# Optimization experiments

Hardware: AMD Instinct MI355X
Metric: run time of the kernel (lower is better)

The kernel has to match this reference:

```python
import jax, jax.numpy as jnp
import numpy as np

K_NN = 3
EPS = 1e-8
MASK_THRESH = 0.5


def _three_nn_interpolate(pts, known, feats):
    """pts: (B,N,3), known: (B,M,3), feats: (B,M,C) -> (B,N,C).
    Squared-distance 3-NN + inverse-distance weighted interpolation
    (pointnet2 three_nn / three_interpolate semantics)."""
    # (B,N,M) squared euclidean distances
    d2 = (jnp.sum(pts * pts, -1)[:, :, None]
          + jnp.sum(known * known, -1)[:, None, :]
          - 2.0 * jnp.einsum('bnd,bmd->bnm', pts, known))
    neg_d, idx = jax.lax.top_k(-d2, K_NN)          # (B,N,3)
    dist = jnp.maximum(-neg_d, 0.0)                # squared dists, clamp fp error
    dist_recip = 1.0 / (dist + EPS)
    weight = dist_recip / jnp.sum(dist_recip, -1, keepdims=True)  # (B,N,3)
    b_idx = jnp.arange(pts.shape[0])[:, None, None]
    gathered = feats[b_idx, idx]                   # (B,N,3,C)
    return jnp.sum(weight[..., None] * gathered, axis=2)  # (B,N,C)


def setup_inputs() -> dict:
    key = jax.random.key(0)
    ks = jax.random.split(key, 10)
    B, N, C = 4, 8192, 32
    M2, M3, M4, Mm = 8192, 4096, 2048, 4096
    sc = 10.0  # spread coords over a realistic metric range
    return {
        'points_mean': jax.random.normal(ks[0], (B, N, 3)) * sc,
        'known2': jax.random.normal(ks[1], (B, M2, 3)) * sc,
        'feats2': jax.random.normal(ks[2], (B, M2, C)),
        'known3': jax.random.normal(ks[3], (B, M3, 3)) * sc,
        'feats3': jax.random.normal(ks[4], (B, M3, C)),
        'known4': jax.random.normal(ks[5], (B, M4, 3)) * sc,
        'feats4': jax.random.normal(ks[6], (B, M4, C)),
        'match_points': jax.random.normal(ks[7], (B, Mm, 3)) * sc,
        'w_fc': jax.random.normal(ks[8], (64, 96)) * 0.1,
        'w_cls': jax.random.normal(ks[9], (1, 64)) * 0.1,
    }


def reference(points_mean, known2, feats2, known3, feats3, known4, feats4,
              match_points, w_fc, w_cls):
    p0 = _three_nn_interpolate(points_mean, known2, feats2)  # (B,N,32)
    p1 = _three_nn_interpolate(points_mean, known3, feats3)
    p2 = _three_nn_interpolate(points_mean, known4, feats4)
    pointwise = jnp.concatenate([p0, p1, p2], axis=-1) @ w_fc.T  # (B,N,64)
    pred_hm = pointwise @ w_cls.T                                 # (B,N,1)
    # GT mask: min distance to match points < 0.5 m
    d2 = (jnp.sum(points_mean * points_mean, -1)[:, :, None]
          + jnp.sum(match_points * match_points, -1)[:, None, :]
          - 2.0 * jnp.einsum('bnd,bmd->bnm', points_mean, match_points))
    min_d = jnp.sqrt(jnp.maximum(jnp.min(d2, axis=-1), 0.0))      # (B,N)
    gt_hm = (min_d < MASK_THRESH).astype(jnp.float32)
    return pred_hm, gt_hm
```

## Files before the change

kernel.cpp:

```cpp
#include <hip/hip_runtime.h>

typedef unsigned int u32;
typedef unsigned long long u64;
typedef float f32x2 __attribute__((ext_vector_type(2)));

#define NB 4
#define NQ 8192
#define MARGIN 0.0625f
#define NBKT 4096

#define OFF_C0   0u
#define OFF_C1   524288u
#define OFF_C2   786432u
#define OFF_CMF  917504u
#define OFF_SKEY 1179648u
#define OFF_BOX  2031616u
#define WS_NEW2  2068480u
#define OFF_CM   917504u
#define WS_OLD   (512u*1024 + 256u*1024 + 128u*1024 + 512u*1024)

struct __align__(32) CP { f32x2 x, y, z, w; };
struct DM { double x, y, z, w; };

__device__ __forceinline__ f32x2 fma2(f32x2 a, f32x2 b, f32x2 c) {
  return __builtin_elementwise_fma(a, b, c);
}

__device__ __forceinline__ void lexins(double& e0d, double& e1d, double& e2d,
                                       int& e0i, int& e1i, int& e2i,
                                       double d, int i) {
  if (d < e2d || (d == e2d && i < e2i)) {
    if (d < e0d || (d == e0d && i < e0i)) {
      e2d = e1d; e2i = e1i; e1d = e0d; e1i = e0i; e0d = d; e0i = i;
    } else if (d < e1d || (d == e1d && i < e1i)) {
      e2d = e1d; e2i = e1i; e1d = d; e1i = i;
    } else {
      e2d = d; e2i = i;
    }
  }
}

__device__ __forceinline__ void ins4(float kv, u32 idx,
                                     float& k0, float& k1, float& k2, float& k3,
                                     u32& i0, u32& i1, u32& i2, u32& i3) {
  if (kv < k3) {
    bool lt0 = kv < k0, lt1 = kv < k1, lt2 = kv < k2;
    k3 = lt2 ? k2 : kv;               i3 = lt2 ? i2 : idx;
    k2 = lt2 ? (lt1 ? k1 : kv) : k2;  i2 = lt2 ? (lt1 ? i1 : idx) : i2;
    k1 = lt1 ? (lt0 ? k0 : kv) : k1;  i1 = lt1 ? (lt0 ? i0 : idx) : i1;
    k0 = lt0 ? kv : k0;               i0 = lt0 ? idx : i0;
  }
}

__device__ __forceinline__ u32 spread10(u32 v) {
  v &= 0x3FFu;
  v = (v | (v << 16)) & 0x030000FFu;
  v = (v | (v << 8))  & 0x0300F00Fu;
  v = (v | (v << 4))  & 0x030C30C3u;
  v = (v | (v << 2))  & 0x09249249u;
  return v;
}
__device__ __forceinline__ u32 morton30(float x, float y, float z) {
  int xi = (int)((x + 64.f) * 8.f);
  int yi = (int)((y + 64.f) * 8.f);
  int zi = (int)((z + 64.f) * 8.f);
  xi = min(max(xi, 0), 1023); yi = min(max(yi, 0), 1023); zi = min(max(zi, 0), 1023);
  return spread10((u32)xi) | (spread10((u32)yi) << 1) | (spread10((u32)zi) << 2);
}

__device__ __forceinline__ size_t skey_abase(int arr) {
  return (arr == 0) ? 0 : (arr == 1) ? 32768 : (arr == 2) ? 49152
        : (arr == 3) ? 57344 : 73728;
}

__global__ __launch_bounds__(512) void prep_csort(
    const float* __restrict__ k2p, const float* __restrict__ k3p,
    const float* __restrict__ k4p, const float* __restrict__ mmp,
    const float* __restrict__ pts, u64* __restrict__ skey) {
  __shared__ u32 hist[NBKT];
  const int arr = blockIdx.x, b = blockIdx.y, tid = threadIdx.x;
  const float* src = (arr == 0) ? k2p : (arr == 1) ? k3p : (arr == 2) ? k4p
                      : (arr == 3) ? mmp : pts;
  const int n = (arr == 0) ? 8192 : (arr == 1) ? 4096 : (arr == 2) ? 2048
                 : (arr == 3) ? 4096 : 8192;
  const float* sb = src + (size_t)b * n * 3;
  u64* skb = skey + skey_abase(arr) + (size_t)b * n;

  for (int i = tid; i < NBKT; i += 512) hist[i] = 0;
  __syncthreads();
  for (int i = tid; i < n; i += 512) {
    u32 k = morton30(sb[3 * i], sb[3 * i + 1], sb[3 * i + 2]);
    atomicAdd(&hist[k >> 18], 1u);
  }
  __syncthreads();
  for (int d = 1; d < NBKT; d <<= 1) {
    for (int i = tid; i < NBKT / (2 * d); i += 512) {
      int idx = (2 * i + 2) * d - 1;
      hist[idx] += hist[idx - d];
    }
    __syncthreads();
  }
  if (tid == 0) hist[NBKT - 1] = 0;
  __syncthreads();
  for (int d = NBKT >> 1; d >= 1; d >>= 1) {
    for (int i = tid; i < NBKT / (2 * d); i += 512) {
      int idx = (2 * i + 2) * d - 1;
      u32 t = hist[idx - d];
      hist[idx - d] = hist[idx];
      hist[idx] += t;
    }
    __syncthreads();
  }
  for (int i = tid; i < n; i += 512) {
    u32 k = morton30(sb[3 * i], sb[3 * i + 1], sb[3 * i + 2]);
    u32 pos = atomicAdd(&hist[k >> 18], 1u);
    skb[pos] = ((u64)k << 32) | (u32)i;
  }
}

__global__ __launch_bounds__(512) void refine_emit(
    const float* __restrict__ k2p, const float* __restrict__ k3p,
    const float* __restrict__ k4p, const float* __restrict__ mmp,
    const float* __restrict__ pts, u64* __restrict__ skey,
    CP* __restrict__ c0, CP* __restrict__ c1, CP* __restrict__ c2,
    float4* __restrict__ cmf, float* __restrict__ boxes) {
  __shared__ u64 ex[512];
  const int widx = blockIdx.x, b = blockIdx.y, tid = threadIdx.x;
  int arr, win;
  if (widx < 16)      { arr = 0; win = widx; }
  else if (widx < 24) { arr = 1; win = widx - 16; }
  else if (widx < 28) { arr = 2; win = widx - 24; }
  else if (widx < 36) { arr = 3; win = widx - 28; }
  else                { arr = 4; win = widx - 36; }
  const float* src = (arr == 0) ? k2p : (arr == 1) ? k3p : (arr == 2) ? k4p
                      : (arr == 3) ? mmp : pts;
  const int n = (arr == 0) ? 8192 : (arr == 1) ? 4096 : (arr == 2) ? 2048
                 : (arr == 3) ? 4096 : 8192;
  u64* skb = skey + skey_abase(arr) + (size_t)b * n;
  const int e = win * 512 + tid;
  u64 v = skb[e];

  for (int k = 2; k <= 512; k <<= 1) {
    for (int j = k >> 1; j > 0; j >>= 1) {
      u64 w;
      if (j < 64) {
        w = __shfl_xor(v, j);
      } else {
        __syncthreads();
        ex[tid] = v;
        __syncthreads();
        w = ex[tid ^ j];
      }
      bool up = (tid & k) == 0;
      bool lower = (tid & j) == 0;
      v = (up == lower) ? (v < w ? v : w) : (v < w ? w : v);
    }
  }
  skb[e] = v;
  if (arr == 4) return;

  u32 p = (u32)v;
  const float* sb = src + (size_t)b * n * 3;
  float x = sb[3 * p], y = sb[3 * p + 1], z = sb[3 * p + 2];
  if (arr < 3) {
    CP* dst = (arr == 0) ? c0 : (arr == 1) ? c1 : c2;
    float* df = (float*)(dst + (size_t)b * (n >> 1) + (e >> 1));
    int sl = e & 1;
    df[sl]     = x;
    df[2 + sl] = y;
    df[4 + sl] = z;
    df[6 + sl] = fmaf(z, z, fmaf(y, y, x * x));
  } else {
    cmf[(size_t)b * 4096 + e] = float4{x, y, z, 0.f};
  }
  float xlo = x, xhi = x, ylo = y, yhi = y, zlo = z, zhi = z;
#pragma unroll
  for (int off = 1; off < 64; off <<= 1) {
    xlo = fminf(xlo, __shfl_xor(xlo, off)); xhi = fmaxf(xhi, __shfl_xor(xhi, off));
    ylo = fminf(ylo, __shfl_xor(ylo, off)); yhi = fmaxf(yhi, __shfl_xor(yhi, off));
    zlo = fminf(zlo, __shfl_xor(zlo, off)); zhi = fmaxf(zhi, __shfl_xor(zhi, off));
  }
  if ((tid & 63) == 0) {
    const int nG = n >> 6, g = e >> 6;
    const int boff = (arr == 0) ? 0 : (arr == 1) ? 512 : (arr == 2) ? 768 : 896;
    float* bx = boxes + ((size_t)boff + (size_t)b * nG + g) * 8;
    bx[0] = xlo; bx[1] = xhi; bx[2] = ylo; bx[3] = yhi; bx[4] = zlo; bx[5] = zhi;
    bx[6] = 0.f; bx[7] = 0.f;
  }
}

__device__ __forceinline__ void scan_pairs32(
    const CP* __restrict__ cg, u32 ebase,
    f32x2 mx2, f32x2 my2, f32x2 mz2,
    float& k0, float& k1, float& k2, float& k3,
    u32& i0, u32& i1, u32& i2, u32& i3) {
#pragma unroll 4
  for (int gg = 0; gg < 32; gg += 4) {
    f32x2 key[4];
#pragma unroll
    for (int u = 0; u < 4; ++u) {
      CP c = cg[gg + u];
      key[u] = fma2(mx2, c.x, fma2(my2, c.y, fma2(mz2, c.z, c.w)));
    }
#pragma unroll
    for (int u = 0; u < 4; ++u) {
      float ka = key[u].x, kb = key[u].y;
      if (fminf(ka, kb) < k3) {
        u32 ib = ebase + (u32)((gg + u) * 2);
        ins4(ka, ib,     k0, k1, k2, k3, i0, i1, i2, i3);
        ins4(kb, ib + 1, k0, k1, k2, k3, i0, i1, i2, i3);
      }
    }
  }
}

struct Smem3 {
  float  box[2304];
  float  qx[64], qy[64], qz[64];
  double qdx[64], qdy[64], qdz[64], qn[64];
  u32    oq[64];
  u32    di[3][64][4][4];
  double mmin[64][8];
  float  wv[96];
  float  wq[64][9];
  u32    iq[64][9];
  float  contrib[64][9];
  float4 stage[8][2][64];
  u32    list[8][32];
};

__global__ __launch_bounds__(512, 2) void fused_sorted2(
    const float* __restrict__ pts,
    const float* __restrict__ f2, const float* __restrict__ f3,
    const float* __restrict__ f4,
    const float* __restrict__ wfc, const float* __restrict__ wcls,
    const CP* __restrict__ c0, const CP* __restrict__ c1,
    const CP* __restrict__ c2, const float4* __restrict__ cmf,
    const u64* __restrict__ skey, const float* __restrict__ boxes,
    float* __restrict__ out) {
  __shared__ Smem3 s;
  const int tid = threadIdx.x;
  const int b = blockIdx.y;
  const int tile = blockIdx.x;
  const int q0 = tile * 64;
  const int qloc = tid & 63;
  const int lane = tid & 63;
  const int wid = __builtin_amdgcn_readfirstlane(tid >> 6);

  {
    float* bf = s.box;
    for (int i = tid; i < 1024; i += 512) bf[i]        = boxes[(size_t)(b * 128) * 8 + i];
    { int i = tid; if (i < 512) bf[1024 + i] = boxes[((size_t)512 + b * 64) * 8 + i]; }
    { int i = tid; if (i < 256) bf[1536 + i] = boxes[((size_t)768 + b * 32) * 8 + i]; }
    { int i = tid; if (i < 512) bf[1792 + i] = boxes[((size_t)896 + b * 64) * 8 + i]; }
  }
  if (tid < 64) {
    u64 kv = skey[73728 + (size_t)b * NQ + q0 + tid];
    u32 p = (u32)kv;
    const float* pb = pts + (size_t)b * NQ * 3;
    float x = pb[3 * p], y = pb[3 * p + 1], z = pb[3 * p + 2];
    s.qx[tid] = x; s.qy[tid] = y; s.qz[tid] = z; s.oq[tid] = p;
    double dx = (double)x, dy = (double)y, dz = (double)z;
    s.qdx[tid] = dx; s.qdy[tid] = dy; s.qdz[tid] = dz;
    s.qn[tid] = (dx * dx + dy * dy) + dz * dz;
  } else if (tid < 160) {
    int t = tid - 64;
    float acc = 0.f;
    for (int j = 0; j < 64; ++j) acc += wcls[j] * wfc[j * 96 + t];
    s.wv[t] = acc;
  }
  __syncthreads();

  const float qx = s.qx[qloc], qy = s.qy[qloc], qz = s.qz[qloc];
  const float qnf = fmaf(qz, qz, fmaf(qy, qy, qx * qx));
  const float fm2x = -2.0f * qx, fm2y = -2.0f * qy, fm2z = -2.0f * qz;
  const double dm2x = -2.0 * s.qdx[qloc];
  const double dm2y = -2.0 * s.qdy[qloc];
  const double dm2z = -2.0 * s.qdz[qloc];

  {
    int lvl, prt, P, lboff;
    if (wid < 4)      { lvl = 0; prt = wid;     P = 4; lboff = 0; }
    else if (wid < 6) { lvl = 1; prt = wid - 4; P = 2; lboff = 128; }
    else              { lvl = 2; prt = wid - 6; P = 2; lboff = 192; }
    const int M  = (lvl == 0) ? 8192 : ((lvl == 1) ? 4096 : 2048);
    const int nG = M >> 6;
    const CP* c4 = ((lvl == 0) ? c0 : ((lvl == 1) ? c1 : c2)) + (((size_t)b * M) >> 1);
    int g0 = (tile * nG) >> 7;
    g0 = (g0 & ~(P - 1)) + prt;

    float k0 = __builtin_inff(), k1 = k0, k2 = k0, k3 = k0;
    u32 i0 = 0, i1 = 0, i2 = 0, i3 = 0;
    const f32x2 mx2 = {fm2x, fm2x}, my2 = {fm2y, fm2y}, mz2 = {fm2z, fm2z};

    scan_pairs32(c4 + (size_t)g0 * 32, (u32)(g0 * 64), mx2, my2, mz2,
                 k0, k1, k2, k3, i0, i1, i2, i3);

    int nl = 0;
    for (int t = 1; t < nG / P; ++t) {
      int g = (g0 + P * t) & (nG - 1);
      const float* bx = &s.box[(lboff + g) * 8];
      float dx = fmaxf(fmaxf(bx[0] - qx, qx - bx[1]), 0.f);
      float dy = fmaxf(fmaxf(bx[2] - qy, qy - bx[3]), 0.f);
      float dz = fmaxf(fmaxf(bx[4] - qz, qz - bx[5]), 0.f);
      float lb = fmaf(dx, dx, fmaf(dy, dy, dz * dz));
      if (__any(lb < qnf + k3 + MARGIN)) {
        if (lane == 0) s.list[wid][nl] = (u32)g;
        ++nl;
      }
    }

    int cur = 0;
    float4 v;
    u32 gcur = 0, gnext = 0;
    if (nl > 0) {
      gcur = s.list[wid][0];
      v = ((const float4*)(c4 + (size_t)gcur * 32))[lane];
    }
    for (int i = 0; i < nl; ++i) {
      s.stage[wid][cur][lane] = v;
      if (i + 1 < nl) {
        gnext = s.list[wid][i + 1];
        v = ((const float4*)(c4 + (size_t)gnext * 32))[lane];
      }
      scan_pairs32((const CP*)&s.stage[wid][cur][0], (u32)(gcur * 64),
                   mx2, my2, mz2, k0, k1, k2, k3, i0, i1, i2, i3);
      gcur = gnext; cur ^= 1;
    }

    s.di[lvl][qloc][prt][0] = i0; s.di[lvl][qloc][prt][1] = i1;
    s.di[lvl][qloc][prt][2] = i2; s.di[lvl][qloc][prt][3] = i3;
  }

  {
    const float4* cmb = cmf + (size_t)b * 4096;
    int gm0 = ((tile * 64) >> 7) & ~7;
    double smin = __builtin_inf();
    for (int t = 0; t < 8; ++t) {
      int g = (gm0 + wid + 8 * t) & 63;
      const float* bx = &s.box[(224 + g) * 8];
      float dx = fmaxf(fmaxf(bx[0] - qx, qx - bx[1]), 0.f);
      float dy = fmaxf(fmaxf(bx[2] - qy, qy - bx[3]), 0.f);
      float dz = fmaxf(fmaxf(bx[4] - qz, qz - bx[5]), 0.f);
      float lb = fmaf(dx, dx, fmaf(dy, dy, dz * dz));
      if (__any(lb < 0.3f)) {
        const float4* c8 = cmb + g * 64;
        for (int j = 0; j < 64; j += 8) {
          double sv[8];
#pragma unroll
          for (int u = 0; u < 8; ++u) {
            float4 cf = c8[j + u];
            double x = (double)cf.x, y = (double)cf.y, z = (double)cf.z;
            double w = fma(z, z, fma(y, y, x * x));
            sv[u] = fma(dm2x, x, fma(dm2y, y, fma(dm2z, z, w)));
          }
          double m01 = fmin(sv[0], sv[1]), m23 = fmin(sv[2], sv[3]);
          double m45 = fmin(sv[4], sv[5]), m67 = fmin(sv[6], sv[7]);
          smin = fmin(smin, fmin(fmin(m01, m23), fmin(m45, m67)));
        }
      }
    }
    s.mmin[qloc][wid] = smin;
  }
  __syncthreads();

  const int gqbase = b * NQ;
  if (tid < 192) {
    const int lvl = __builtin_amdgcn_readfirstlane(tid >> 6);
    const int q = tid & 63;
    const int M  = (lvl == 0) ? 8192 : ((lvl == 1) ? 4096 : 2048);
    const int np = (lvl == 0) ? 4 : 2;
    const CP* c4 = ((lvl == 0) ? c0 : ((lvl == 1) ? c1 : c2)) + (((size_t)b * M) >> 1);
    const u64* skl = skey + ((lvl == 0) ? 0 : (lvl == 1) ? 32768 : 49152)
                     + (size_t)b * M;
    const double qdx = s.qdx[q], qdy = s.qdy[q], qdz = s.qdz[q], qn = s.qn[q];
    double e0 = __builtin_inf(), e1 = e0, e2 = e0;
    int i0 = 0, i1 = 0, i2 = 0;
    for (int h = 0; h < np; ++h) {
#pragma unroll
      for (int r = 0; r < 4; ++r) {
        int sidx = (int)s.di[lvl][q][h][r];
        CP cc = c4[sidx >> 1];
        bool hi = sidx & 1;
        double x = (double)(hi ? cc.x.y : cc.x.x);
        double y = (double)(hi ? cc.y.y : cc.y.x);
        double z = (double)(hi ? cc.z.y : cc.z.x);
        int orig = (int)(u32)skl[sidx];
        double kn2 = (x * x + y * y) + z * z;
        double dot = (qdx * x + qdy * y) + qdz * z;
        double d2 = (qn + kn2) - 2.0 * dot;
        lexins(e0, e1, e2, i0, i1, i2, d2, orig);
      }
    }
    double d0 = fmax(e0, 0.0), d1 = fmax(e1, 0.0), d2v = fmax(e2, 0.0);
    double r0 = 1.0 / (d0 + 1e-8);
    double r1 = 1.0 / (d1 + 1e-8);
    double r2 = 1.0 / (d2v + 1e-8);
    double sum = (r0 + r1) + r2;
    s.wq[q][lvl * 3 + 0] = (float)(r0 / sum); s.iq[q][lvl * 3 + 0] = (u32)i0;
    s.wq[q][lvl * 3 + 1] = (float)(r1 / sum); s.iq[q][lvl * 3 + 1] = (u32)i1;
    s.wq[q][lvl * 3 + 2] = (float)(r2 / sum); s.iq[q][lvl * 3 + 2] = (u32)i2;
  } else if (tid < 256) {
    const int q = tid - 192;
    double sm = s.mmin[q][0];
#pragma unroll
    for (int p = 1; p < 8; ++p) sm = fmin(sm, s.mmin[q][p]);
    double dm = s.qn[q] + sm;
    out[NB * NQ + gqbase + (int)s.oq[q]] = (dm < 0.25) ? 1.0f : 0.0f;
  }
  __syncthreads();

  for (int item = tid; item < 576; item += 512) {
    const int q = item & 63, j = item >> 6;
    const int lvl = j / 3;
    const float* fp = (lvl == 0) ? f2 : ((lvl == 1) ? f3 : f4);
    const int M = (lvl == 0) ? 8192 : ((lvl == 1) ? 4096 : 2048);
    const float4* row = (const float4*)(fp + ((size_t)b * M + s.iq[q][j]) * 32);
    const float* wvp = s.wv + lvl * 32;
    float acc = 0.f;
#pragma unroll
    for (int v = 0; v < 8; ++v) {
      float4 r = row[v];
      acc += wvp[4 * v] * r.x + wvp[4 * v + 1] * r.y
           + wvp[4 * v + 2] * r.z + wvp[4 * v + 3] * r.w;
    }
    s.contrib[q][j] = s.wq[q][j] * acc;
  }
  __syncthreads();
  if (tid < 64) {
    const float* c = s.contrib[tid];
    float l0 = (c[0] + c[1]) + c[2];
    float l1 = (c[3] + c[4]) + c[5];
    float l2 = (c[6] + c[7]) + c[8];
    out[gqbase + (int)s.oq[tid]] = (l0 + l1) + l2;
  }
}

__global__ __launch_bounds__(256) void prep_kernel(
    const float* __restrict__ k2p, const float* __restrict__ k3p,
    const float* __restrict__ k4p, const float* __restrict__ mmp,
    CP* __restrict__ c0, CP* __restrict__ c1,
    CP* __restrict__ c2, DM* __restrict__ cm) {
  int r = blockIdx.y;
  int i = blockIdx.x * 256 + threadIdx.x;
  if (r < 3) {
    const float* src = (r == 0) ? k2p : ((r == 1) ? k3p : k4p);
    CP* dst = (r == 0) ? c0 : ((r == 1) ? c1 : c2);
    int pairs = (r == 0) ? NB * 4096 : ((r == 1) ? NB * 2048 : NB * 1024);
    if (i >= pairs) return;
    const float* p = src + (size_t)i * 6;
    float x0 = p[0], y0 = p[1], z0 = p[2];
    float x1 = p[3], y1 = p[4], z1 = p[5];
    CP c;
    c.x = f32x2{x0, x1}; c.y = f32x2{y0, y1}; c.z = f32x2{z0, z1};
    c.w = f32x2{fmaf(z0, z0, fmaf(y0, y0, x0 * x0)),
                fmaf(z1, z1, fmaf(y1, y1, x1 * x1))};
    dst[i] = c;
  } else {
    if (i >= NB * 4096) return;
    double x = (double)mmp[3 * i], y = (double)mmp[3 * i + 1], z = (double)mmp[3 * i + 2];
    DM d = {x, y, z, fma(z, z, fma(y, y, x * x))};
    cm[i] = d;
  }
}

template <bool PREP>
__device__ __forceinline__ void scan_nn(
    const CP* __restrict__ cp, const float* __restrict__ raw,
    int gstart, int L, float m2x, float m2y, float m2z,
    float* kk, u32* ii) {
  float k0 = __builtin_inff(), k1 = k0, k2 = k0, k3 = k0;
  u32 i0 = 0, i1 = 0, i2 = 0, i3 = 0;
  if (PREP) {
    const f32x2 mx2 = {m2x, m2x}, my2 = {m2y, m2y}, mz2 = {m2z, m2z};
    const int G = L >> 1;
#pragma unroll 2
    for (int g = 0; g < G; g += 4) {
      f32x2 key[4];
#pragma unroll
      for (int u = 0; u < 4; ++u) {
        CP c = cp[g + u];
        key[u] = fma2(mx2, c.x, fma2(my2, c.y, fma2(mz2, c.z, c.w)));
      }
#pragma unroll
      for (int u = 0; u < 4; ++u) {
        float ka = key[u].x, kb = key[u].y;
        if (fminf(ka, kb) < k3) {
          u32 ib = (u32)(gstart + 2 * (g + u));
          ins4(ka, ib,     k0, k1, k2, k3, i0, i1, i2, i3);
          ins4(kb, ib + 1, k0, k1, k2, k3, i0, i1, i2, i3);
        }
      }
    }
  } else {
    for (int j = 0; j < L; j += 8) {
      float key[8];
#pragma unroll
      for (int u = 0; u < 8; ++u) {
        const float* p = raw + (size_t)(gstart + j + u) * 3;
        float x = p[0], y = p[1], z = p[2];
        float n2 = fmaf(z, z, fmaf(y, y, x * x));
        key[u] = fmaf(m2x, x, fmaf(m2y, y, fmaf(m2z, z, n2)));
      }
#pragma unroll
      for (int u = 0; u < 8; ++u)
        ins4(key[u], (u32)(gstart + j + u), k0, k1, k2, k3, i0, i1, i2, i3);
    }
  }
  kk[0] = k0; kk[1] = k1; kk[2] = k2; kk[3] = k3;
  ii[0] = i0; ii[1] = i1; ii[2] = i2; ii[3] = i3;
}

template <bool PREP>
__device__ __forceinline__ double scan_mask(
    const DM* __restrict__ c8, const float* __restrict__ raw,
    int gstart, int L, double m2x, double m2y, double m2z) {
  double smin = __builtin_inf();
  if (PREP) {
    for (int j = 0; j < L; j += 8) {
      double sv[8];
#pragma unroll
      for (int u = 0; u < 8; ++u) {
        DM c = c8[gstart + j + u];
        sv[u] = fma(m2x, c.x, fma(m2y, c.y, fma(m2z, c.z, c.w)));
      }
      double m01 = fmin(sv[0], sv[1]), m23 = fmin(sv[2], sv[3]);
      double m45 = fmin(sv[4], sv[5]), m67 = fmin(sv[6], sv[7]);
      smin = fmin(smin, fmin(fmin(m01, m23), fmin(m45, m67)));
    }
  } else {
    for (int j = 0; j < L; j += 4) {
#pragma unroll
      for (int u = 0; u < 4; ++u) {
        const float* p = raw + (size_t)(gstart + j + u) * 3;
        double x = (double)p[0], y = (double)p[1], z = (double)p[2];
        double kn = fma(z, z, fma(y, y, x * x));
        smin = fmin(smin, fma(m2x, x, fma(m2y, y, fma(m2z, z, kn))));
      }
    }
  }
  return smin;
}

struct Smem {
  float  qx[64], qy[64], qz[64];
  double qdx[64], qdy[64], qdz[64], qn[64];
  float  dk[3][64][4][4];
  u32    di[3][64][4][4];
  double mmin[64][8];
  float  wv[96];
  float  part[64][3];
};

template <bool PREP>
__global__ __launch_bounds__(512, 2) void fused_kernel(
    const float* __restrict__ pts,
    const float* __restrict__ k2p, const float* __restrict__ f2,
    const float* __restrict__ k3p, const float* __restrict__ f3,
    const float* __restrict__ k4p, const float* __restrict__ f4,
    const float* __restrict__ mmp,
    const float* __restrict__ wfc, const float* __restrict__ wcls,
    const CP* __restrict__ c0, const CP* __restrict__ c1,
    const CP* __restrict__ c2, const DM* __restrict__ cm,
    float* __restrict__ out) {
  __shared__ Smem s;
  const int tid = threadIdx.x;
  const int b = blockIdx.y;
  const int q0 = blockIdx.x * 64;
  const int qloc = tid & 63;
  const int wid = __builtin_amdgcn_readfirstlane(tid >> 6);

  if (tid < 64) {
    int gq = b * NQ + q0 + tid;
    float x = pts[3 * gq], y = pts[3 * gq + 1], z = pts[3 * gq + 2];
    s.qx[tid] = x; s.qy[tid] = y; s.qz[tid] = z;
    double dx = (double)x, dy = (double)y, dz = (double)z;
    s.qdx[tid] = dx; s.qdy[tid] = dy; s.qdz[tid] = dz;
    s.qn[tid] = (dx * dx + dy * dy) + dz * dz;
  } else if (tid < 160) {
    int t = tid - 64;
    float acc = 0.f;
    for (int j = 0; j < 64; ++j) acc += wcls[j] * wfc[j * 96 + t];
    s.wv[t] = acc;
  }
  __syncthreads();

  const float fm2x = -2.0f * s.qx[qloc];
  const float fm2y = -2.0f * s.qy[qloc];
  const float fm2z = -2.0f * s.qz[qloc];
  const double dm2x = -2.0 * s.qdx[qloc];
  const double dm2y = -2.0 * s.qdy[qloc];
  const double dm2z = -2.0 * s.qdz[qloc];

  {
    int lvl, prt, gstart, glen;
    if (wid < 4)      { lvl = 0; prt = wid;     gstart = wid * 2048;       glen = 2048; }
    else if (wid < 6) { lvl = 1; prt = wid - 4; gstart = (wid - 4) * 2048; glen = 2048; }
    else              { lvl = 2; prt = wid - 6; gstart = (wid - 6) * 1024; glen = 1024; }
    const CP* c4 = (lvl == 0) ? c0 : ((lvl == 1) ? c1 : c2);
    const float* raw = (lvl == 0) ? k2p : ((lvl == 1) ? k3p : k4p);
    const int      M = (lvl == 0) ? 8192 : ((lvl == 1) ? 4096 : 2048);
    float kk[4]; u32 ii[4];
    scan_nn<PREP>(c4 + (PREP ? (((size_t)b * M + gstart) >> 1) : 0),
                  raw + (size_t)b * M * 3,
                  gstart, glen, fm2x, fm2y, fm2z, kk, ii);
#pragma unroll
    for (int r = 0; r < 4; ++r) {
      s.dk[lvl][qloc][prt][r] = kk[r];
      s.di[lvl][qloc][prt][r] = ii[r];
    }
    int mstart, mlen;
    if (wid < 6) { mstart = wid * 256; mlen = 256; }
    else         { mstart = 1536 + (wid - 6) * 1280; mlen = 1280; }
    s.mmin[qloc][wid] = scan_mask<PREP>(cm + (PREP ? (size_t)b * 4096 : 0),
                                        mmp + (size_t)b * 4096 * 3,
                                        mstart, mlen, dm2x, dm2y, dm2z);
  }
  __syncthreads();

  const int gqbase = b * NQ + q0;
  if (tid < 192) {
    const int lvl = __builtin_amdgcn_readfirstlane(tid >> 6);
    const int q = tid & 63;
    const float* kp = (lvl == 0) ? k2p : ((lvl == 1) ? k3p : k4p);
    const int    M  = (lvl == 0) ? 8192 : ((lvl == 1) ? 4096 : 2048);
    const int    np = (lvl == 0) ? 4 : 2;
    const double qdx = s.qdx[q], qdy = s.qdy[q], qdz = s.qdz[q], qn = s.qn[q];
    double e0 = __builtin_inf(), e1 = e0, e2 = e0;
    int i0 = 0, i1 = 0, i2 = 0;
    for (int h = 0; h < np; ++h) {
#pragma unroll
      for (int r = 0; r < 4; ++r) {
        int idx = (int)s.di[lvl][q][h][r];
        const float* c = kp + ((size_t)b * M + idx) * 3;
        double x = (double)c[0], y = (double)c[1], z = (double)c[2];
        double kn2 = (x * x + y * y) + z * z;
        double dot = (qdx * x + qdy * y) + qdz * z;
        double d2 = (qn + kn2) - 2.0 * dot;
        lexins(e0, e1, e2, i0, i1, i2, d2, idx);
      }
    }
    double d0 = fmax(e0, 0.0), d1 = fmax(e1, 0.0), d2v = fmax(e2, 0.0);
    double r0 = 1.0 / (d0 + 1e-8);
    double r1 = 1.0 / (d1 + 1e-8);
    double r2 = 1.0 / (d2v + 1e-8);
    double sum = (r0 + r1) + r2;
    float wa = (float)(r0 / sum), wb = (float)(r1 / sum), wc = (float)(r2 / sum);
    const float* fp = (lvl == 0) ? f2 : ((lvl == 1) ? f3 : f4);
    const float* g0 = fp + ((size_t)b * M + i0) * 32;
    const float* g1 = fp + ((size_t)b * M + i1) * 32;
    const float* g2 = fp + ((size_t)b * M + i2) * 32;
    float acc = 0.f;
#pragma unroll
    for (int wd = 0; wd < 32; ++wd) {
      float v = (wa * g0[wd] + wb * g1[wd]) + wc * g2[wd];
      acc += s.wv[lvl * 32 + wd] * v;
    }
    s.part[q][lvl] = acc;
  } else if (tid < 256) {
    const int q = tid - 192;
    double sm = s.mmin[q][0];
#pragma unroll
    for (int p = 1; p < 8; ++p) sm = fmin(sm, s.mmin[q][p]);
    double dm = s.qn[q] + sm;
    out[NB * NQ + gqbase + q] = (dm < 0.25) ? 1.0f : 0.0f;
  }
  __syncthreads();
  if (tid < 64) {
    float pred = (s.part[tid][0] + s.part[tid][1]) + s.part[tid][2];
    out[gqbase + tid] = pred;
  }
}

extern "C" void kernel_launch(void* const* d_in, const int* in_sizes, int n_in,
                              void* d_out, int out_size, void* d_ws, size_t ws_size,
                              hipStream_t stream) {
  const float* pts    = (const float*)d_in[0];
  const float* known2 = (const float*)d_in[1];
  const float* feats2 = (const float*)d_in[2];
  const float* known3 = (const float*)d_in[3];
  const float* feats3 = (const float*)d_in[4];
  const float* known4 = (const float*)d_in[5];
  const float* feats4 = (const float*)d_in[6];
  const float* match  = (const float*)d_in[7];
  const float* wfc    = (const float*)d_in[8];
  const float* wcls   = (const float*)d_in[9];

  char* ws = (char*)d_ws;
  CP* c0 = (CP*)(ws + OFF_C0);
  CP* c1 = (CP*)(ws + OFF_C1);
  CP* c2 = (CP*)(ws + OFF_C2);

  if (ws_size >= WS_NEW2) {
    float4* cmf = (float4*)(ws + OFF_CMF);
    u64* skey = (u64*)(ws + OFF_SKEY);
    float* boxes = (float*)(ws + OFF_BOX);
    hipLaunchKernelGGL(prep_csort, dim3(5, NB), dim3(512), 0, stream,
                       known2, known3, known4, match, pts, skey);
    hipLaunchKernelGGL(refine_emit, dim3(52, NB), dim3(512), 0, stream,
                       known2, known3, known4, match, pts, skey,
                       c0, c1, c2, cmf, boxes);
    hipLaunchKernelGGL(fused_sorted2, dim3(NQ / 64, NB), dim3(512), 0, stream,
                       pts, feats2, feats3, feats4, wfc, wcls,
                       c0, c1, c2, cmf, skey, boxes, (float*)d_out);
  } else if (ws_size >= WS_OLD) {
    DM* cm = (DM*)(ws + OFF_CM);
    hipLaunchKernelGGL(prep_kernel, dim3(64, 4), dim3(256), 0, stream,
                       known2, known3, known4, match, c0, c1, c2, cm);
    hipLaunchKernelGGL(HIP_KERNEL_NAME(fused_kernel<true>), dim3(NQ / 64, NB),
                       dim3(512), 0, stream, pts, known2, feats2, known3, feats3,
                       known4, feats4, match, wfc, wcls, c0, c1, c2, cm,
                       (float*)d_out);
  } else {
    DM* cm = (DM*)(ws + OFF_CM);
    hipLaunchKernelGGL(HIP_KERNEL_NAME(fused_kernel<false>), dim3(NQ / 64, NB),
                       dim3(512), 0, stream, pts, known2, feats2, known3, feats3,
                       known4, feats4, match, wfc, wcls, c0, c1, c2, cm,
                       (float*)d_out);
  }
}
```

Measured before the change: 237.3 us.

## Split query tiles to 32 queries per 256-thread block with half-wave candidate splitting

The main fused kernel now handles 32 queries per 256-thread block instead of 64 per 512, and each wave's two halves scan different 16-pair halves of a candidate group. Group pruning is re-checked against the current best distance just before each group is loaded, and match points are stored in the packed pair layout, so the mask pass uses a float prefilter before the double-precision check. The histogram-sort kernel moves to 1024 threads. This trades more blocks and extra voting for less serial scan work per lane and better occupancy, at the cost of more per-block setup such as the box loads and weight folding.

```diff
diff --git a/kernel.cpp b/kernel.cpp
--- a/kernel.cpp
+++ b/kernel.cpp
@@ -12,7 +12,7 @@
 #define OFF_C0   0u
 #define OFF_C1   524288u
 #define OFF_C2   786432u
-#define OFF_CMF  917504u
+#define OFF_CMP  917504u
 #define OFF_SKEY 1179648u
 #define OFF_BOX  2031616u
 #define WS_NEW2  2068480u
@@ -73,7 +73,7 @@
         : (arr == 3) ? 57344 : 73728;
 }
 
-__global__ __launch_bounds__(512) void prep_csort(
+__global__ __launch_bounds__(1024) void prep_csort(
     const float* __restrict__ k2p, const float* __restrict__ k3p,
     const float* __restrict__ k4p, const float* __restrict__ mmp,
     const float* __restrict__ pts, u64* __restrict__ skey) {
@@ -86,15 +86,15 @@
   const float* sb = src + (size_t)b * n * 3;
   u64* skb = skey + skey_abase(arr) + (size_t)b * n;
 
-  for (int i = tid; i < NBKT; i += 512) hist[i] = 0;
-  __syncthreads();
-  for (int i = tid; i < n; i += 512) {
+  for (int i = tid; i < NBKT; i += 1024) hist[i] = 0;
+  __syncthreads();
+  for (int i = tid; i < n; i += 1024) {
     u32 k = morton30(sb[3 * i], sb[3 * i + 1], sb[3 * i + 2]);
     atomicAdd(&hist[k >> 18], 1u);
   }
   __syncthreads();
   for (int d = 1; d < NBKT; d <<= 1) {
-    for (int i = tid; i < NBKT / (2 * d); i += 512) {
+    for (int i = tid; i < NBKT / (2 * d); i += 1024) {
       int idx = (2 * i + 2) * d - 1;
       hist[idx] += hist[idx - d];
     }
@@ -103,7 +103,7 @@
   if (tid == 0) hist[NBKT - 1] = 0;
   __syncthreads();
   for (int d = NBKT >> 1; d >= 1; d >>= 1) {
-    for (int i = tid; i < NBKT / (2 * d); i += 512) {
+    for (int i = tid; i < NBKT / (2 * d); i += 1024) {
       int idx = (2 * i + 2) * d - 1;
       u32 t = hist[idx - d];
       hist[idx - d] = hist[idx];
@@ -111,7 +111,7 @@
     }
     __syncthreads();
   }
-  for (int i = tid; i < n; i += 512) {
+  for (int i = tid; i < n; i += 1024) {
     u32 k = morton30(sb[3 * i], sb[3 * i + 1], sb[3 * i + 2]);
     u32 pos = atomicAdd(&hist[k >> 18], 1u);
     skb[pos] = ((u64)k << 32) | (u32)i;
@@ -123,7 +123,7 @@
     const float* __restrict__ k4p, const float* __restrict__ mmp,
     const float* __restrict__ pts, u64* __restrict__ skey,
     CP* __restrict__ c0, CP* __restrict__ c1, CP* __restrict__ c2,
-    float4* __restrict__ cmf, float* __restrict__ boxes) {
+    CP* __restrict__ cmp, float* __restrict__ boxes) {
   __shared__ u64 ex[512];
   const int widx = blockIdx.x, b = blockIdx.y, tid = threadIdx.x;
   int arr, win;
@@ -162,16 +162,14 @@
   u32 p = (u32)v;
   const float* sb = src + (size_t)b * n * 3;
   float x = sb[3 * p], y = sb[3 * p + 1], z = sb[3 * p + 2];
-  if (arr < 3) {
-    CP* dst = (arr == 0) ? c0 : (arr == 1) ? c1 : c2;
+  {
+    CP* dst = (arr == 0) ? c0 : (arr == 1) ? c1 : (arr == 2) ? c2 : cmp;
     float* df = (float*)(dst + (size_t)b * (n >> 1) + (e >> 1));
     int sl = e & 1;
     df[sl]     = x;
     df[2 + sl] = y;
     df[4 + sl] = z;
     df[6 + sl] = fmaf(z, z, fmaf(y, y, x * x));
-  } else {
-    cmf[(size_t)b * 4096 + e] = float4{x, y, z, 0.f};
   }
   float xlo = x, xhi = x, ylo = y, yhi = y, zlo = z, zhi = z;
 #pragma unroll
@@ -189,13 +187,13 @@
   }
 }
 
-__device__ __forceinline__ void scan_pairs32(
+__device__ __forceinline__ void scan_pairs16(
     const CP* __restrict__ cg, u32 ebase,
     f32x2 mx2, f32x2 my2, f32x2 mz2,
     float& k0, float& k1, float& k2, float& k3,
     u32& i0, u32& i1, u32& i2, u32& i3) {
 #pragma unroll 4
-  for (int gg = 0; gg < 32; gg += 4) {
+  for (int gg = 0; gg < 16; gg += 4) {
     f32x2 key[4];
 #pragma unroll
     for (int u = 0; u < 4; ++u) {
@@ -214,48 +212,49 @@
   }
 }
 
-struct Smem3 {
+struct Smem4 {
   float  box[2304];
-  float  qx[64], qy[64], qz[64];
-  double qdx[64], qdy[64], qdz[64], qn[64];
-  u32    oq[64];
-  u32    di[3][64][4][4];
-  double mmin[64][8];
+  float  qx[32], qy[32], qz[32];
+  double qdx[32], qdy[32], qdz[32], qn[32];
+  u32    oq[32];
+  u32    di[3][32][4][4];
+  double mmin[32][8];
   float  wv[96];
-  float  wq[64][9];
-  u32    iq[64][9];
-  float  contrib[64][9];
-  float4 stage[8][2][64];
-  u32    list[8][32];
+  float  wq[32][9];
+  u32    iq[32][9];
+  float  contrib[32][9];
+  float4 stage[4][2][64];
+  u32    list[4][64];
 };
 
-__global__ __launch_bounds__(512, 2) void fused_sorted2(
+__global__ __launch_bounds__(256, 4) void fused_sorted3(
     const float* __restrict__ pts,
     const float* __restrict__ f2, const float* __restrict__ f3,
     const float* __restrict__ f4,
     const float* __restrict__ wfc, const float* __restrict__ wcls,
     const CP* __restrict__ c0, const CP* __restrict__ c1,
-    const CP* __restrict__ c2, const float4* __restrict__ cmf,
+    const CP* __restrict__ c2, const CP* __restrict__ cmp,
     const u64* __restrict__ skey, const float* __restrict__ boxes,
     float* __restrict__ out) {
-  __shared__ Smem3 s;
+  __shared__ Smem4 s;
   const int tid = threadIdx.x;
   const int b = blockIdx.y;
   const int tile = blockIdx.x;
-  const int q0 = tile * 64;
-  const int qloc = tid & 63;
   const int lane = tid & 63;
+  const int q = tid & 31;
+  const int h = (tid >> 5) & 1;
   const int wid = __builtin_amdgcn_readfirstlane(tid >> 6);
 
-  {
-    float* bf = s.box;
-    for (int i = tid; i < 1024; i += 512) bf[i]        = boxes[(size_t)(b * 128) * 8 + i];
-    { int i = tid; if (i < 512) bf[1024 + i] = boxes[((size_t)512 + b * 64) * 8 + i]; }
-    { int i = tid; if (i < 256) bf[1536 + i] = boxes[((size_t)768 + b * 32) * 8 + i]; }
-    { int i = tid; if (i < 512) bf[1792 + i] = boxes[((size_t)896 + b * 64) * 8 + i]; }
-  }
-  if (tid < 64) {
-    u64 kv = skey[73728 + (size_t)b * NQ + q0 + tid];
+  for (int i = tid; i < 2304; i += 256) {
+    int src;
+    if (i < 1024)      src = (b * 128) * 8 + i;
+    else if (i < 1536) src = (512 + b * 64) * 8 + (i - 1024);
+    else if (i < 1792) src = (768 + b * 32) * 8 + (i - 1536);
+    else               src = (896 + b * 64) * 8 + (i - 1792);
+    s.box[i] = boxes[src];
+  }
+  if (tid < 32) {
+    u64 kv = skey[73728 + (size_t)b * NQ + tile * 32 + tid];
     u32 p = (u32)kv;
     const float* pb = pts + (size_t)b * NQ * 3;
     float x = pb[3 * p], y = pb[3 * p + 1], z = pb[3 * p + 2];
@@ -263,42 +262,41 @@
     double dx = (double)x, dy = (double)y, dz = (double)z;
     s.qdx[tid] = dx; s.qdy[tid] = dy; s.qdz[tid] = dz;
     s.qn[tid] = (dx * dx + dy * dy) + dz * dz;
-  } else if (tid < 160) {
-    int t = tid - 64;
+  } else if (tid < 128) {
+    int t = tid - 32;
     float acc = 0.f;
     for (int j = 0; j < 64; ++j) acc += wcls[j] * wfc[j * 96 + t];
     s.wv[t] = acc;
   }
   __syncthreads();
 
-  const float qx = s.qx[qloc], qy = s.qy[qloc], qz = s.qz[qloc];
+  const float qx = s.qx[q], qy = s.qy[q], qz = s.qz[q];
   const float qnf = fmaf(qz, qz, fmaf(qy, qy, qx * qx));
   const float fm2x = -2.0f * qx, fm2y = -2.0f * qy, fm2z = -2.0f * qz;
-  const double dm2x = -2.0 * s.qdx[qloc];
-  const double dm2y = -2.0 * s.qdy[qloc];
-  const double dm2z = -2.0 * s.qdz[qloc];
+  const double qdx = s.qdx[q], qdy = s.qdy[q], qdz = s.qdz[q], qn = s.qn[q];
+  const f32x2 mx2 = {fm2x, fm2x}, my2 = {fm2y, fm2y}, mz2 = {fm2z, fm2z};
 
   {
-    int lvl, prt, P, lboff;
-    if (wid < 4)      { lvl = 0; prt = wid;     P = 4; lboff = 0; }
-    else if (wid < 6) { lvl = 1; prt = wid - 4; P = 2; lboff = 128; }
-    else              { lvl = 2; prt = wid - 6; P = 2; lboff = 192; }
-    const int M  = (lvl == 0) ? 8192 : ((lvl == 1) ? 4096 : 2048);
-    const int nG = M >> 6;
+    int lvl, part, nG, g0, stride, nvote, lboff;
+    if (wid < 2)      { lvl = 0; nG = 128; stride = 2; nvote = 63;
+                        g0 = (((tile * 128) >> 8) & ~1) | wid;
+                        part = wid * 2 + h; lboff = 0; }
+    else if (wid == 2){ lvl = 1; nG = 64;  stride = 1; nvote = 63;
+                        g0 = (tile * 64) >> 8; part = h; lboff = 128; }
+    else              { lvl = 2; nG = 32;  stride = 1; nvote = 31;
+                        g0 = (tile * 32) >> 8; part = h; lboff = 192; }
+    const int M = 8192 >> lvl;
     const CP* c4 = ((lvl == 0) ? c0 : ((lvl == 1) ? c1 : c2)) + (((size_t)b * M) >> 1);
-    int g0 = (tile * nG) >> 7;
-    g0 = (g0 & ~(P - 1)) + prt;
 
     float k0 = __builtin_inff(), k1 = k0, k2 = k0, k3 = k0;
     u32 i0 = 0, i1 = 0, i2 = 0, i3 = 0;
-    const f32x2 mx2 = {fm2x, fm2x}, my2 = {fm2y, fm2y}, mz2 = {fm2z, fm2z};
-
-    scan_pairs32(c4 + (size_t)g0 * 32, (u32)(g0 * 64), mx2, my2, mz2,
-                 k0, k1, k2, k3, i0, i1, i2, i3);
+
+    scan_pairs16(c4 + g0 * 32 + h * 16, (u32)(g0 * 64 + h * 32),
+                 mx2, my2, mz2, k0, k1, k2, k3, i0, i1, i2, i3);
 
     int nl = 0;
-    for (int t = 1; t < nG / P; ++t) {
-      int g = (g0 + P * t) & (nG - 1);
+    for (int t = 1; t <= nvote; ++t) {
+      int g = (g0 + stride * t) & (nG - 1);
       const float* bx = &s.box[(lboff + g) * 8];
       float dx = fmaxf(fmaxf(bx[0] - qx, qx - bx[1]), 0.f);
       float dy = fmaxf(fmaxf(bx[2] - qy, qy - bx[3]), 0.f);
@@ -310,76 +308,92 @@
       }
     }
 
-    int cur = 0;
+    auto accept = [&](int g) -> bool {
+      const float* bx = &s.box[(lboff + g) * 8];
+      float dx = fmaxf(fmaxf(bx[0] - qx, qx - bx[1]), 0.f);
+      float dy = fmaxf(fmaxf(bx[2] - qy, qy - bx[3]), 0.f);
+      float dz = fmaxf(fmaxf(bx[4] - qz, qz - bx[5]), 0.f);
+      float lb = fmaf(dx, dx, fmaf(dy, dy, dz * dz));
+      return __any(lb < qnf + k3 + MARGIN);
+    };
+    int ip = 0, cur = 0, gcur = -1;
     float4 v;
-    u32 gcur = 0, gnext = 0;
-    if (nl > 0) {
-      gcur = s.list[wid][0];
-      v = ((const float4*)(c4 + (size_t)gcur * 32))[lane];
-    }
-    for (int i = 0; i < nl; ++i) {
+    while (ip < nl) {
+      int g = (int)s.list[wid][ip++];
+      if (accept(g)) { gcur = g; v = ((const float4*)(c4 + (size_t)g * 32))[lane]; break; }
+    }
+    while (gcur >= 0) {
       s.stage[wid][cur][lane] = v;
-      if (i + 1 < nl) {
-        gnext = s.list[wid][i + 1];
-        v = ((const float4*)(c4 + (size_t)gnext * 32))[lane];
-      }
-      scan_pairs32((const CP*)&s.stage[wid][cur][0], (u32)(gcur * 64),
+      int gn = -1;
+      while (ip < nl) {
+        int g = (int)s.list[wid][ip++];
+        if (accept(g)) { gn = g; break; }
+      }
+      if (gn >= 0) v = ((const float4*)(c4 + (size_t)gn * 32))[lane];
+      const CP* sg = (const CP*)&s.stage[wid][cur][0];
+      scan_pairs16(sg + h * 16, (u32)(gcur * 64 + h * 32),
                    mx2, my2, mz2, k0, k1, k2, k3, i0, i1, i2, i3);
-      gcur = gnext; cur ^= 1;
-    }
-
-    s.di[lvl][qloc][prt][0] = i0; s.di[lvl][qloc][prt][1] = i1;
-    s.di[lvl][qloc][prt][2] = i2; s.di[lvl][qloc][prt][3] = i3;
+      gcur = gn; cur ^= 1;
+    }
+
+    s.di[lvl][q][part][0] = i0; s.di[lvl][q][part][1] = i1;
+    s.di[lvl][q][part][2] = i2; s.di[lvl][q][part][3] = i3;
   }
 
   {
-    const float4* cmb = cmf + (size_t)b * 4096;
-    int gm0 = ((tile * 64) >> 7) & ~7;
-    double smin = __builtin_inf();
-    for (int t = 0; t < 8; ++t) {
-      int g = (gm0 + wid + 8 * t) & 63;
+    const CP* cmb = cmp + (size_t)b * 2048;
+    int gm0 = tile >> 2;
+    double dmin = __builtin_inf();
+    for (int t = 0; t < 16; ++t) {
+      int g = (gm0 + wid + 4 * t) & 63;
       const float* bx = &s.box[(224 + g) * 8];
       float dx = fmaxf(fmaxf(bx[0] - qx, qx - bx[1]), 0.f);
       float dy = fmaxf(fmaxf(bx[2] - qy, qy - bx[3]), 0.f);
       float dz = fmaxf(fmaxf(bx[4] - qz, qz - bx[5]), 0.f);
       float lb = fmaf(dx, dx, fmaf(dy, dy, dz * dz));
-      if (__any(lb < 0.3f)) {
-        const float4* c8 = cmb + g * 64;
-        for (int j = 0; j < 64; j += 8) {
-          double sv[8];
-#pragma unroll
-          for (int u = 0; u < 8; ++u) {
-            float4 cf = c8[j + u];
-            double x = (double)cf.x, y = (double)cf.y, z = (double)cf.z;
-            double w = fma(z, z, fma(y, y, x * x));
-            sv[u] = fma(dm2x, x, fma(dm2y, y, fma(dm2z, z, w)));
+      if (__any(lb < 0.26f)) {
+        const CP* cg = cmb + g * 32 + h * 16;
+#pragma unroll 4
+        for (int p = 0; p < 16; ++p) {
+          CP c = cg[p];
+          f32x2 key = fma2(mx2, c.x, fma2(my2, c.y, fma2(mz2, c.z, c.w)));
+          if (fminf(key.x, key.y) + qnf < 0.252f) {
+            {
+              double x = (double)c.x.x, y = (double)c.y.x, z = (double)c.z.x;
+              double kn2 = (x * x + y * y) + z * z;
+              double dot = (qdx * x + qdy * y) + qdz * z;
+              dmin = fmin(dmin, (qn + kn2) - 2.0 * dot);
+            }
+            {
+              double x = (double)c.x.y, y = (double)c.y.y, z = (double)c.z.y;
+              double kn2 = (x * x + y * y) + z * z;
+              double dot = (qdx * x + qdy * y) + qdz * z;
+              dmin = fmin(dmin, (qn + kn2) - 2.0 * dot);
+            }
           }
-          double m01 = fmin(sv[0], sv[1]), m23 = fmin(sv[2], sv[3]);
-          double m45 = fmin(sv[4], sv[5]), m67 = fmin(sv[6], sv[7]);
-          smin = fmin(smin, fmin(fmin(m01, m23), fmin(m45, m67)));
         }
       }
     }
-    s.mmin[qloc][wid] = smin;
+    s.mmin[q][wid * 2 + h] = dmin;
   }
   __syncthreads();
 
   const int gqbase = b * NQ;
-  if (tid < 192) {
-    const int lvl = __builtin_amdgcn_readfirstlane(tid >> 6);
-    const int q = tid & 63;
-    const int M  = (lvl == 0) ? 8192 : ((lvl == 1) ? 4096 : 2048);
+  if (tid < 96) {
+    const int lvl = tid >> 5;
+    const int qq = tid & 31;
+    const int M  = 8192 >> lvl;
     const int np = (lvl == 0) ? 4 : 2;
     const CP* c4 = ((lvl == 0) ? c0 : ((lvl == 1) ? c1 : c2)) + (((size_t)b * M) >> 1);
     const u64* skl = skey + ((lvl == 0) ? 0 : (lvl == 1) ? 32768 : 49152)
                      + (size_t)b * M;
-    const double qdx = s.qdx[q], qdy = s.qdy[q], qdz = s.qdz[q], qn = s.qn[q];
+    const double tqdx = s.qdx[qq], tqdy = s.qdy[qq], tqdz = s.qdz[qq], tqn = s.qn[qq];
     double e0 = __builtin_inf(), e1 = e0, e2 = e0;
-    int i0 = 0, i1 = 0, i2 = 0;
-    for (int h = 0; h < np; ++h) {
+    int j0 = 0, j1 = 0, j2 = 0;
+    for (int hh = 0; hh < np; ++hh) {
 #pragma unroll
       for (int r = 0; r < 4; ++r) {
-        int sidx = (int)s.di[lvl][q][h][r];
+        int sidx = (int)s.di[lvl][qq][hh][r];
         CP cc = c4[sidx >> 1];
         bool hi = sidx & 1;
         double x = (double)(hi ? cc.x.y : cc.x.x);
@@ -387,9 +401,9 @@
         double z = (double)(hi ? cc.z.y : cc.z.x);
         int orig = (int)(u32)skl[sidx];
         double kn2 = (x * x + y * y) + z * z;
-        double dot = (qdx * x + qdy * y) + qdz * z;
-        double d2 = (qn + kn2) - 2.0 * dot;
-        lexins(e0, e1, e2, i0, i1, i2, d2, orig);
+        double dot = (tqdx * x + tqdy * y) + tqdz * z;
+        double d2 = (tqn + kn2) - 2.0 * dot;
+        lexins(e0, e1, e2, j0, j1, j2, d2, orig);
       }
     }
     double d0 = fmax(e0, 0.0), d1 = fmax(e1, 0.0), d2v = fmax(e2, 0.0);
@@ -397,25 +411,24 @@
     double r1 = 1.0 / (d1 + 1e-8);
     double r2 = 1.0 / (d2v + 1e-8);
     double sum = (r0 + r1) + r2;
-    s.wq[q][lvl * 3 + 0] = (float)(r0 / sum); s.iq[q][lvl * 3 + 0] = (u32)i0;
-    s.wq[q][lvl * 3 + 1] = (float)(r1 / sum); s.iq[q][lvl * 3 + 1] = (u32)i1;
-    s.wq[q][lvl * 3 + 2] = (float)(r2 / sum); s.iq[q][lvl * 3 + 2] = (u32)i2;
-  } else if (tid < 256) {
-    const int q = tid - 192;
-    double sm = s.mmin[q][0];
-#pragma unroll
-    for (int p = 1; p < 8; ++p) sm = fmin(sm, s.mmin[q][p]);
-    double dm = s.qn[q] + sm;
-    out[NB * NQ + gqbase + (int)s.oq[q]] = (dm < 0.25) ? 1.0f : 0.0f;
-  }
-  __syncthreads();
-
-  for (int item = tid; item < 576; item += 512) {
-    const int q = item & 63, j = item >> 6;
+    s.wq[qq][lvl * 3 + 0] = (float)(r0 / sum); s.iq[qq][lvl * 3 + 0] = (u32)j0;
+    s.wq[qq][lvl * 3 + 1] = (float)(r1 / sum); s.iq[qq][lvl * 3 + 1] = (u32)j1;
+    s.wq[qq][lvl * 3 + 2] = (float)(r2 / sum); s.iq[qq][lvl * 3 + 2] = (u32)j2;
+  } else if (tid < 128) {
+    const int qq = tid - 96;
+    double dm = s.mmin[qq][0];
+#pragma unroll
+    for (int p = 1; p < 8; ++p) dm = fmin(dm, s.mmin[qq][p]);
+    out[NB * NQ + gqbase + (int)s.oq[qq]] = (dm < 0.25) ? 1.0f : 0.0f;
+  }
+  __syncthreads();
+
+  for (int item = tid; item < 288; item += 256) {
+    const int qq = item & 31, j = item >> 5;
     const int lvl = j / 3;
     const float* fp = (lvl == 0) ? f2 : ((lvl == 1) ? f3 : f4);
-    const int M = (lvl == 0) ? 8192 : ((lvl == 1) ? 4096 : 2048);
-    const float4* row = (const float4*)(fp + ((size_t)b * M + s.iq[q][j]) * 32);
+    const int M = 8192 >> lvl;
+    const float4* row = (const float4*)(fp + ((size_t)b * M + s.iq[qq][j]) * 32);
     const float* wvp = s.wv + lvl * 32;
     float acc = 0.f;
 #pragma unroll
@@ -424,10 +437,10 @@
       acc += wvp[4 * v] * r.x + wvp[4 * v + 1] * r.y
            + wvp[4 * v + 2] * r.z + wvp[4 * v + 3] * r.w;
     }
-    s.contrib[q][j] = s.wq[q][j] * acc;
-  }
-  __syncthreads();
-  if (tid < 64) {
+    s.contrib[qq][j] = s.wq[qq][j] * acc;
+  }
+  __syncthreads();
+  if (tid < 32) {
     const float* c = s.contrib[tid];
     float l0 = (c[0] + c[1]) + c[2];
     float l1 = (c[3] + c[4]) + c[5];
@@ -692,17 +705,17 @@
   CP* c2 = (CP*)(ws + OFF_C2);
 
   if (ws_size >= WS_NEW2) {
-    float4* cmf = (float4*)(ws + OFF_CMF);
+    CP* cmp = (CP*)(ws + OFF_CMP);
     u64* skey = (u64*)(ws + OFF_SKEY);
     float* boxes = (float*)(ws + OFF_BOX);
-    hipLaunchKernelGGL(prep_csort, dim3(5, NB), dim3(512), 0, stream,
+    hipLaunchKernelGGL(prep_csort, dim3(5, NB), dim3(1024), 0, stream,
                        known2, known3, known4, match, pts, skey);
     hipLaunchKernelGGL(refine_emit, dim3(52, NB), dim3(512), 0, stream,
                        known2, known3, known4, match, pts, skey,
-                       c0, c1, c2, cmf, boxes);
-    hipLaunchKernelGGL(fused_sorted2, dim3(NQ / 64, NB), dim3(512), 0, stream,
+                       c0, c1, c2, cmp, boxes);
+    hipLaunchKernelGGL(fused_sorted3, dim3(NQ / 32, NB), dim3(256), 0, stream,
                        pts, feats2, feats3, feats4, wfc, wcls,
-                       c0, c1, c2, cmf, skey, boxes, (float*)d_out);
+                       c0, c1, c2, cmp, skey, boxes, (float*)d_out);
   } else if (ws_size >= WS_OLD) {
     DM* cm = (DM*)(ws + OFF_CM);
     hipLaunchKernelGGL(prep_kernel, dim3(64, 4), dim3(256), 0, stream,
```

New measurement: 229.9 us. 3.1% less time.
